# Kernel optimization log

Measured on AMD Instinct MI355X. Metric: run time of the kernel, lower is better.

The kernel has to match this reference:

```python
import jax
jax.config.update("jax_enable_x64", True)
import jax.numpy as jnp
import numpy as np

EPS = 1e-10
NODES = [
    {"type": 0, "feature_idx": 0},
    {"type": 0, "feature_idx": 1},
    {"type": 0, "feature_idx": 2},
    {"type": 0, "feature_idx": 3},
    {"type": 1, "value": 2.5},
    {"type": 2, "unary_op": 0, "left_child": 0, "p": 1.0, "omega": 1.3, "phi": 0.2, "amplitude": 1.1},
    {"type": 2, "unary_op": 1, "left_child": 1, "p": 2.0, "omega": 1.0, "phi": 0.0, "amplitude": 1.0},
    {"type": 2, "unary_op": 1, "left_child": 2, "p": 1.7, "omega": 1.0, "phi": 0.0, "amplitude": 1.0},
    {"type": 2, "unary_op": 3, "left_child": 3, "p": 1.0, "omega": 0.5, "phi": 0.0, "amplitude": 1.0},
    {"type": 2, "unary_op": 4, "left_child": 0, "p": 1.0, "omega": 1.0, "phi": 0.0, "amplitude": 1.0},
    {"type": 2, "unary_op": 2, "left_child": 1, "p": 3.0, "omega": 1.0, "phi": 0.0, "amplitude": 1.0},
    {"type": 3, "binary_op": 0, "left_child": 5, "right_child": 6, "beta": 1.0, "gamma": 1.0, "tau": 1.0},
    {"type": 3, "binary_op": 0, "left_child": 7, "right_child": 8, "beta": 1.0, "gamma": -1.0, "tau": 1.0},
    {"type": 3, "binary_op": 0, "left_child": 9, "right_child": 10, "beta": 2.0, "gamma": 1.0, "tau": 1.0},
    {"type": 3, "binary_op": 0, "left_child": 11, "right_child": 4, "beta": 2.0, "gamma": -1.0, "tau": 1.0},
    {"type": 3, "binary_op": 1, "left_child": 12, "right_child": 13, "beta": 1.0, "gamma": 1.0, "tau": 1.0},
    {"type": 3, "binary_op": 2, "left_child": 14, "right_child": 15, "beta": 1.0, "gamma": 1.0, "tau": 0.5},
    {"type": 2, "unary_op": 0, "left_child": 16, "p": 1.0, "omega": 0.7, "phi": -0.3, "amplitude": 0.9},
    {"type": 3, "binary_op": 0, "left_child": 17, "right_child": 11, "beta": 1.0, "gamma": 1.0, "tau": 1.0},
]

def _safe_div(l, r):
    return l / (jnp.abs(r) + EPS) * jnp.sign(r)

def _eval_graph(x, output_weights, output_bias):
    x = x.astype(jnp.float64)  # mirrors x.double()
    n = x.shape[0]
    outs = []
    for node in NODES:
        t = node["type"]
        if t == 0:  # input
            out = x[:, node["feature_idx"]]
        elif t == 1:  # constant
            out = jnp.full((n,), node["value"], dtype=jnp.float64)
        elif t == 2:  # unary
            child = outs[node["left_child"]]
            op = node["unary_op"]
            p, omega, phi, amp = node["p"], node["omega"], node["phi"], node["amplitude"]
            if op == 0:  # periodic
                out = amp * jnp.sin(omega * child + phi)
            elif op == 1:  # power (sign-safe)
                abs_pow = (jnp.abs(child) + EPS) ** p
                p_round = round(p)
                is_even = 1.0 if (abs(p - p_round) < 1e-6 and int(p_round) % 2 == 0) else 0.0
                out = (1.0 - is_even) * (jnp.sign(child) * abs_pow) + is_even * abs_pow
            elif op == 2:  # int pow
                k = int(min(max(round(p), 2), 6))
                out = child ** k
            elif op == 3:  # exp
                out = jnp.exp(jnp.clip(omega * child + phi, -20.0, 20.0))
            elif op == 4:  # log
                out = jnp.log(jnp.abs(child) + EPS)
            else:
                out = child
        elif t == 3:  # binary
            l = outs[node["left_child"]]
            r = outs[node["right_child"]]
            op = node["binary_op"]
            beta, gamma = node["beta"], node["gamma"]
            if op == 0:  # arithmetic (branch resolves statically on fixed buffers)
                if beta < 1.5:
                    out = l + r if gamma > 0 else l - r
                elif gamma > 0:
                    out = l * r
                else:
                    out = _safe_div(l, r)
            elif op == 1:  # division
                out = _safe_div(l, r)
            else:  # aggregation: soft-max-weighted mean
                tau = node["tau"]
                local_tau = tau if abs(tau) >= 1e-3 else 1e-3
                m = jnp.maximum(l, r)
                el = jnp.exp((l - m) / local_tau)
                er = jnp.exp((r - m) / local_tau)
                out = (l * el + r * er) / (el + er)
        else:
            out = jnp.zeros((n,), dtype=jnp.float64)
        out = jnp.clip(out, -1e6, 1e6)
        out = jnp.where(jnp.isfinite(out), out, 0.0)
        outs.append(out)
    stacked = jnp.stack(outs, axis=0)  # (K, N)
    w = output_weights.astype(jnp.float64)
    return w @ stacked + output_bias.astype(jnp.float64)


def setup_inputs() -> dict:
    key = jax.random.key(0)
    k1, k2, k3 = jax.random.split(key, 3)
    x = jax.random.normal(k1, (2_000_000, 8), dtype=jnp.float32)
    output_weights = jax.random.normal(k2, (19,), dtype=jnp.float32) * 0.2
    output_bias = jax.random.normal(k3, (), dtype=jnp.float32) * 0.1
    return {"x": x, "output_weights": output_weights, "output_bias": output_bias}


def reference(x, output_weights, output_bias):
    return _eval_graph(x, output_weights, output_bias)
```

## Files before the change

### kernel.cpp

```cpp
#include <hip/hip_runtime.h>
#include <math.h>

__device__ __forceinline__ double dexp(double t) {
    const double LOG2E  = 1.4426950408889634;
    const double LN2_HI = 6.93147180369123816490e-01;
    const double LN2_LO = 1.90821492927058770002e-10;
    double kd = __builtin_floor(t * LOG2E + 0.5);
    double f  = (t - kd * LN2_HI) - kd * LN2_LO;
    double p = 1.0 / 362880.0;
    p = p * f + 1.0 / 40320.0;
    p = p * f + 1.0 / 5040.0;
    p = p * f + 1.0 / 720.0;
    p = p * f + 1.0 / 120.0;
    p = p * f + 1.0 / 24.0;
    p = p * f + 1.0 / 6.0;
    p = p * f + 0.5;
    p = p * f + 1.0;
    p = p * f + 1.0;
    long long k = (long long)kd;
    return __longlong_as_double(__double_as_longlong(p) + (k << 52));
}
__device__ __forceinline__ double dlog(double y) {
    long long b = __double_as_longlong(y);
    int e = (int)((b >> 52) & 0x7FF) - 1022;
    double m = __longlong_as_double((b & 0x000FFFFFFFFFFFFFLL) | 0x3FE0000000000000LL);
    if (m < 0.7071067811865476) { m = m + m; e -= 1; }
    double s  = (m - 1.0) / (m + 1.0);
    double s2 = s * s;
    double p = 1.0 / 15.0;
    p = p * s2 + 1.0 / 13.0;
    p = p * s2 + 1.0 / 11.0;
    p = p * s2 + 1.0 / 9.0;
    p = p * s2 + 1.0 / 7.0;
    p = p * s2 + 1.0 / 5.0;
    p = p * s2 + 1.0 / 3.0;
    p = p * s2 + 1.0;
    return (double)e * 0.6931471805599453 + 2.0 * s * p;
}

__device__ __forceinline__ float fast_sin(float th) {
    float rev = th * 0.15915494309189535f;
    rev = rev - floorf(rev);
    return __builtin_amdgcn_sinf(rev);
}

struct W {
    float w0, w1, w2, w3;
    float c5, c6, c7, c8;
    float w9, w10, w13, w15, w16, c17;
    float base;
};

__device__ __forceinline__ float eval_row(const W& q, float x0, float x1, float x2, float x3) {
    float n5 = 1.1f * fast_sin(fmaf(1.3f, x0, 0.2f));
    float t6 = fabsf(x1) + 1e-10f;
    float n6 = t6 * t6;
    float y2 = fabsf(x2) + 1e-10f;
    float sgn2 = (x2 > 0.f) ? 1.f : ((x2 < 0.f) ? -1.f : 0.f);
    float n7 = sgn2 * __expf(1.7f * __logf(y2));
    float n8 = __expf(fminf(fmaxf(0.5f * x3, -20.f), 20.f));
    float n9 = __logf(fabsf(x0) + 1e-10f);
    float n10 = x1 * x1 * x1;
    float n11 = n5 + n6;
    float n12 = n7 - n8;
    float n13 = n9 * n10;
    float n14 = 0.4f * n11;

    float a13 = fabsf(n13);
    float sgn13 = (n13 > 0.f) ? 1.f : ((n13 < 0.f) ? -1.f : 0.f);
    float n15 = n12 * __builtin_amdgcn_rcpf(a13 + 1e-10f) * sgn13;
    n15 = fminf(fmaxf(n15, -1.0e6f), 1.0e6f);

    bool flag = a13 < 1e-7f;
    if (flag) {
        float s13 = (x1 == 0.f) ? 0.f
                  : (((fabsf(x0) >= 1.0f) == (x1 > 0.f)) ? 1.f : -1.f);
        n15 = copysignf(1.0e6f, n12) * s13;
    }
    bool x0n1 = fabsf(fabsf(x0) - 1.0f) < 1e-4f;
    if ((flag && fabsf(n12) < 0.25f) || x0n1) {
        double n7d = (double)sgn2 * dexp(1.7 * dlog(fabs((double)x2) + 1e-10));
        double n8d = dexp(fmin(fmax(0.5 * (double)x3, -20.0), 20.0));
        double n9d = dlog(fabs((double)x0) + 1e-10);
        double x1d = (double)x1;
        double n12d = n7d - n8d;
        double n13d = n9d * (x1d * x1d * x1d);
        double sd = (n13d > 0.0) ? 1.0 : ((n13d < 0.0) ? -1.0 : 0.0);
        double rr = n12d / (fabs(n13d) + 1e-10) * sd;
        n15 = (float)fmin(fmax(rr, -1.0e6), 1.0e6);
    }

    float d = n14 - n15;
    float s = __builtin_amdgcn_rcpf(1.0f + __expf(-2.0f * d));
    float n16 = n15 + d * s;
    float n17 = 0.9f * fast_sin(fmaf(0.7f, n16, -0.3f));

    float r = q.base;
    r += q.w0 * x0 + q.w1 * x1 + q.w2 * x2 + q.w3 * x3;
    r += q.c5 * n5 + q.c6 * n6 + q.c7 * n7 + q.c8 * n8;
    r += q.w9 * n9 + q.w10 * n10 + q.w13 * n13;
    r += q.w15 * n15 + q.w16 * n16 + q.c17 * n17;
    return r;
}

__global__ void __launch_bounds__(256) graph_eval(
    const float4* __restrict__ x4,
    const float*  __restrict__ w,
    const float*  __restrict__ bias,
    float2*       __restrict__ out2,
    int nhalf)
{
    int j = blockIdx.x * blockDim.x + threadIdx.x;
    if (j >= nhalf) return;

    float4 a = x4[4 * j];
    float4 b = x4[4 * j + 2];

    W q;
    float c11 = w[11] + 0.4f * w[14] + w[18];
    q.w0 = w[0];  q.w1 = w[1];  q.w2 = w[2];  q.w3 = w[3];
    q.c5 = w[5] + c11;  q.c6 = w[6] + c11;
    q.c7 = w[7] + w[12];  q.c8 = w[8] - w[12];
    q.w9 = w[9];  q.w10 = w[10];  q.w13 = w[13];
    q.w15 = w[15];  q.w16 = w[16];  q.c17 = w[17] + w[18];
    q.base = bias[0] + 2.5f * w[4];

    float r0 = eval_row(q, a.x, a.y, a.z, a.w);
    float r1 = eval_row(q, b.x, b.y, b.z, b.w);
    out2[j] = make_float2(r0, r1);
}

extern "C" void kernel_launch(void* const* d_in, const int* in_sizes, int n_in,
                              void* d_out, int out_size, void* d_ws, size_t ws_size,
                              hipStream_t stream) {
    const float4* x  = (const float4*)d_in[0];
    const float*  w  = (const float*)d_in[1];
    const float*  b  = (const float*)d_in[2];
    float2* out = (float2*)d_out;
    int nhalf = out_size / 2;
    int block = 256;
    int grid = (nhalf + block - 1) / block;
    graph_eval<<<grid, block, 0, stream>>>(x, w, b, out, nhalf);
}
```

Baseline: 17.94 us.

## Switch to grid-stride one-row-per-thread loop with folded constants

Replaces the two-rows-per-thread kernel with a fixed grid of 2048 blocks running a grid-stride loop over single rows. The output is written as scalar floats, and the weight constants are hoisted out of the loop. Sine pre-scaling, log/exp base conversions and amplitude factors are folded into the constants so exp2/log2 and sin are called directly. This trades per-thread ILP and vectorized float2 stores for fewer launched threads and amortized weight loads, and it changes the memory access pattern to one float4 load per row.

After: 18.86 us. 5.2% more time.

```diff
diff --git a/kernel.cpp b/kernel.cpp
--- a/kernel.cpp
+++ b/kernel.cpp
@@ -38,96 +38,85 @@
     return (double)e * 0.6931471805599453 + 2.0 * s * p;
 }
 
-__device__ __forceinline__ float fast_sin(float th) {
-    float rev = th * 0.15915494309189535f;
-    rev = rev - floorf(rev);
-    return __builtin_amdgcn_sinf(rev);
-}
-
-struct W {
-    float w0, w1, w2, w3;
-    float c5, c6, c7, c8;
-    float w9, w10, w13, w15, w16, c17;
-    float base;
-};
-
-__device__ __forceinline__ float eval_row(const W& q, float x0, float x1, float x2, float x3) {
-    float n5 = 1.1f * fast_sin(fmaf(1.3f, x0, 0.2f));
-    float t6 = fabsf(x1) + 1e-10f;
-    float n6 = t6 * t6;
-    float y2 = fabsf(x2) + 1e-10f;
-    float sgn2 = (x2 > 0.f) ? 1.f : ((x2 < 0.f) ? -1.f : 0.f);
-    float n7 = sgn2 * __expf(1.7f * __logf(y2));
-    float n8 = __expf(fminf(fmaxf(0.5f * x3, -20.f), 20.f));
-    float n9 = __logf(fabsf(x0) + 1e-10f);
-    float n10 = x1 * x1 * x1;
-    float n11 = n5 + n6;
-    float n12 = n7 - n8;
-    float n13 = n9 * n10;
-    float n14 = 0.4f * n11;
-
-    float a13 = fabsf(n13);
-    float sgn13 = (n13 > 0.f) ? 1.f : ((n13 < 0.f) ? -1.f : 0.f);
-    float n15 = n12 * __builtin_amdgcn_rcpf(a13 + 1e-10f) * sgn13;
-    n15 = fminf(fmaxf(n15, -1.0e6f), 1.0e6f);
-
-    bool flag = a13 < 1e-7f;
-    if (flag) {
-        float s13 = (x1 == 0.f) ? 0.f
-                  : (((fabsf(x0) >= 1.0f) == (x1 > 0.f)) ? 1.f : -1.f);
-        n15 = copysignf(1.0e6f, n12) * s13;
-    }
-    bool x0n1 = fabsf(fabsf(x0) - 1.0f) < 1e-4f;
-    if ((flag && fabsf(n12) < 0.25f) || x0n1) {
-        double n7d = (double)sgn2 * dexp(1.7 * dlog(fabs((double)x2) + 1e-10));
-        double n8d = dexp(fmin(fmax(0.5 * (double)x3, -20.0), 20.0));
-        double n9d = dlog(fabs((double)x0) + 1e-10);
-        double x1d = (double)x1;
-        double n12d = n7d - n8d;
-        double n13d = n9d * (x1d * x1d * x1d);
-        double sd = (n13d > 0.0) ? 1.0 : ((n13d < 0.0) ? -1.0 : 0.0);
-        double rr = n12d / (fabs(n13d) + 1e-10) * sd;
-        n15 = (float)fmin(fmax(rr, -1.0e6), 1.0e6);
-    }
-
-    float d = n14 - n15;
-    float s = __builtin_amdgcn_rcpf(1.0f + __expf(-2.0f * d));
-    float n16 = n15 + d * s;
-    float n17 = 0.9f * fast_sin(fmaf(0.7f, n16, -0.3f));
-
-    float r = q.base;
-    r += q.w0 * x0 + q.w1 * x1 + q.w2 * x2 + q.w3 * x3;
-    r += q.c5 * n5 + q.c6 * n6 + q.c7 * n7 + q.c8 * n8;
-    r += q.w9 * n9 + q.w10 * n10 + q.w13 * n13;
-    r += q.w15 * n15 + q.w16 * n16 + q.c17 * n17;
-    return r;
-}
+#define INV2PI 0.15915494309189535f
+#define LOG2E  1.4426950408889634f
+#define LN2    0.6931471805599453f
 
 __global__ void __launch_bounds__(256) graph_eval(
     const float4* __restrict__ x4,
     const float*  __restrict__ w,
     const float*  __restrict__ bias,
-    float2*       __restrict__ out2,
-    int nhalf)
+    float*        __restrict__ out,
+    int n)
 {
-    int j = blockIdx.x * blockDim.x + threadIdx.x;
-    if (j >= nhalf) return;
+    float c11 = w[11] + 0.4f * w[14] + w[18];
+    float c5  = 1.1f * (w[5] + c11);
+    float c6  = w[6] + c11;
+    float c7  = w[7] + w[12];
+    float c8  = w[8] - w[12];
+    float c17 = 0.9f * (w[17] + w[18]);
+    float base = bias[0] + 2.5f * w[4];
+    float w0 = w[0], w1 = w[1], w2 = w[2], w3 = w[3];
+    float w9 = w[9], w10 = w[10], w13 = w[13], w15 = w[15], w16 = w[16];
 
-    float4 a = x4[4 * j];
-    float4 b = x4[4 * j + 2];
+    int stride = gridDim.x * blockDim.x;
+    for (int i = blockIdx.x * blockDim.x + threadIdx.x; i < n; i += stride) {
+        float4 v = x4[2 * i];
+        float x0 = v.x, x1 = v.y, x2 = v.z, x3 = v.w;
 
-    W q;
-    float c11 = w[11] + 0.4f * w[14] + w[18];
-    q.w0 = w[0];  q.w1 = w[1];  q.w2 = w[2];  q.w3 = w[3];
-    q.c5 = w[5] + c11;  q.c6 = w[6] + c11;
-    q.c7 = w[7] + w[12];  q.c8 = w[8] - w[12];
-    q.w9 = w[9];  q.w10 = w[10];  q.w13 = w[13];
-    q.w15 = w[15];  q.w16 = w[16];  q.c17 = w[17] + w[18];
-    q.base = bias[0] + 2.5f * w[4];
+        float r5 = fmaf(1.3f * INV2PI, x0, 0.2f * INV2PI);
+        float s5 = __builtin_amdgcn_sinf(r5 - floorf(r5));
+        float t6 = fabsf(x1) + 1e-10f;
+        float n6 = t6 * t6;
+        float y2 = fabsf(x2) + 1e-10f;
+        float m7 = exp2f(1.7f * log2f(y2));
+        float n7 = copysignf(m7, x2);
+        float n8 = exp2f(fminf(fmaxf(x3 * (0.5f * LOG2E), -20.f * LOG2E), 20.f * LOG2E));
+        float n9 = LN2 * log2f(fabsf(x0) + 1e-10f);
+        float n10 = x1 * x1 * x1;
 
-    float r0 = eval_row(q, a.x, a.y, a.z, a.w);
-    float r1 = eval_row(q, b.x, b.y, b.z, b.w);
-    out2[j] = make_float2(r0, r1);
+        float n12 = n7 - n8;
+        float n13 = n9 * n10;
+        float n14 = fmaf(0.44f, s5, 0.4f * n6);
+
+        float a13 = fabsf(n13);
+        float sgn13 = (n13 > 0.f) ? 1.f : ((n13 < 0.f) ? -1.f : 0.f);
+        float n15 = n12 * __builtin_amdgcn_rcpf(a13 + 1e-10f) * sgn13;
+        n15 = fminf(fmaxf(n15, -1.0e6f), 1.0e6f);
+
+        bool flag = a13 < 1e-7f;
+        if (flag) {
+            float s13 = (x1 == 0.f) ? 0.f
+                      : (((fabsf(x0) >= 1.0f) == (x1 > 0.f)) ? 1.f : -1.f);
+            n15 = copysignf(1.0e6f, n12) * s13;
+        }
+        bool x0n1 = fabsf(fabsf(x0) - 1.0f) < 1e-4f;
+        if ((flag && fabsf(n12) < 0.25f) || x0n1) {
+            double m7d = dexp(1.7 * dlog(fabs((double)x2) + 1e-10));
+            double n7d = (x2 > 0.f) ? m7d : ((x2 < 0.f) ? -m7d : 0.0);
+            double n8d = dexp(fmin(fmax(0.5 * (double)x3, -20.0), 20.0));
+            double n9d = dlog(fabs((double)x0) + 1e-10);
+            double x1d = (double)x1;
+            double n12d = n7d - n8d;
+            double n13d = n9d * (x1d * x1d * x1d);
+            double sd = (n13d > 0.0) ? 1.0 : ((n13d < 0.0) ? -1.0 : 0.0);
+            double rr = n12d / (fabs(n13d) + 1e-10) * sd;
+            n15 = (float)fmin(fmax(rr, -1.0e6), 1.0e6);
+        }
+
+        float d = n14 - n15;
+        float s = __builtin_amdgcn_rcpf(1.0f + exp2f(-2.0f * LOG2E * d));
+        float n16 = fmaf(d, s, n15);
+        float r17 = fmaf(0.7f * INV2PI, n16, -0.3f * INV2PI);
+        float s17 = __builtin_amdgcn_sinf(r17 - floorf(r17));
+
+        float r = base;
+        r += w0 * x0 + w1 * x1 + w2 * x2 + w3 * x3;
+        r += c5 * s5 + c6 * n6 + c7 * n7 + c8 * n8;
+        r += w9 * n9 + w10 * n10 + w13 * n13;
+        r += w15 * n15 + w16 * n16 + c17 * s17;
+        out[i] = r;
+    }
 }
 
 extern "C" void kernel_launch(void* const* d_in, const int* in_sizes, int n_in,
@@ -136,9 +125,9 @@
     const float4* x  = (const float4*)d_in[0];
     const float*  w  = (const float*)d_in[1];
     const float*  b  = (const float*)d_in[2];
-    float2* out = (float2*)d_out;
-    int nhalf = out_size / 2;
+    float* out = (float*)d_out;
+    int n = out_size;
     int block = 256;
-    int grid = (nhalf + block - 1) / block;
-    graph_eval<<<grid, block, 0, stream>>>(x, w, b, out, nhalf);
+    int grid = 2048;
+    graph_eval<<<grid, block, 0, stream>>>(x, w, b, out, n);
 }
```
